# Performance work log

Hardware: AMD Instinct MI355X
Metric: run time of the kernel (lower is better)

The kernel has to match this reference:

```python
import jax, jax.numpy as jnp
import numpy as np

D, NH, L, P, FF = 256, 8, 3, 4, 1024
DH = D // NH
EPS = 1e-5

def _ln(x, g, b):
    m = jnp.mean(x, axis=-1, keepdims=True)
    v = jnp.mean((x - m) ** 2, axis=-1, keepdims=True)
    return (x - m) * jax.lax.rsqrt(v + EPS) * g + b

def _bilinear(value, loc, Hl, Wl):
    # value: [B,NH,Nl,DH]; loc (x,y) in [0,1]: [B,N,NH,P,2]; grid_sample align_corners=False, zero padding
    B, N = loc.shape[0], loc.shape[1]
    x = loc[..., 0] * Wl - 0.5
    y = loc[..., 1] * Hl - 0.5
    x0 = jnp.floor(x)
    y0 = jnp.floor(y)
    lx, ly = x - x0, y - y0
    x0 = x0.astype(jnp.int32)
    y0 = y0.astype(jnp.int32)

    def gather(xi, yi):
        valid = ((xi >= 0) & (xi < Wl) & (yi >= 0) & (yi < Hl)).astype(value.dtype)
        idx = jnp.clip(yi, 0, Hl - 1) * Wl + jnp.clip(xi, 0, Wl - 1)  # [B,N,NH,P]
        idx = idx.transpose(0, 2, 1, 3).reshape(B, NH, N * P, 1)
        v = jnp.take_along_axis(value, idx, axis=2)  # [B,NH,N*P,DH]
        v = v.reshape(B, NH, N, P, DH).transpose(0, 2, 1, 3, 4)  # [B,N,NH,P,DH]
        return v * valid[..., None]

    v00 = gather(x0, y0)
    v01 = gather(x0 + 1, y0)
    v10 = gather(x0, y0 + 1)
    v11 = gather(x0 + 1, y0 + 1)
    return (v00 * ((1 - lx) * (1 - ly))[..., None] + v01 * (lx * (1 - ly))[..., None]
            + v10 * ((1 - lx) * ly)[..., None] + v11 * (lx * ly)[..., None])

def _forward(query, p3, p4, p5, Wv, bv, Woff, boff, Wattn, battn, Wref, bref, Wo, bo,
             W1, b1, W2, b2, g1, be1, g2, be2, shapes):
    B, N, _ = query.shape
    off = (query @ Woff + boff).reshape(B, N, NH, L, P, 2)
    aw = jax.nn.softmax((query @ Wattn + battn).reshape(B, N, NH, L * P), axis=-1).reshape(B, N, NH, L, P)
    ref = jax.nn.sigmoid(query @ Wref + bref)[:, :, None, None, :]  # [B,N,1,1,2]
    out = jnp.zeros((B, N, NH, DH), query.dtype)
    for l, (feat, (Hl, Wl)) in enumerate(zip((p3, p4, p5), shapes)):
        val = (feat @ Wv + bv).reshape(B, Hl * Wl, NH, DH).transpose(0, 2, 1, 3)  # [B,NH,Nl,DH]
        loc = ref + off[:, :, :, l] / jnp.array([Wl, Hl], query.dtype)  # offsets normalized by (W,H)
        samp = _bilinear(val, loc, Hl, Wl)  # [B,N,NH,P,DH]
        out = out + jnp.einsum('bnhp,bnhpd->bnhd', aw[:, :, :, l], samp)
    attn_out = out.reshape(B, N, D) @ Wo + bo
    q = _ln(query + attn_out, g1, be1)  # residual + norm1 (dropout=eval identity)
    ffn = jax.nn.gelu(q @ W1 + b1, approximate=False) @ W2 + b2
    return _ln(q + ffn, g2, be2)

def setup_inputs():
    key = jax.random.key(0)
    ks = jax.random.split(key, 12)
    B = 4
    H3, W3, H4, W4, H5, W5 = 100, 100, 50, 50, 25, 25
    N = H3 * W3 + H4 * W4 + H5 * W5
    s = 0.02
    f32 = jnp.float32
    return dict(
        query=jax.random.normal(ks[0], (B, N, D), f32),
        p3=jax.random.normal(ks[1], (B, H3 * W3, D), f32),
        p4=jax.random.normal(ks[2], (B, H4 * W4, D), f32),
        p5=jax.random.normal(ks[3], (B, H5 * W5, D), f32),
        Wv=jax.random.normal(ks[4], (D, D), f32) * s, bv=jnp.zeros((D,), f32),
        Woff=jax.random.normal(ks[5], (D, NH * L * P * 2), f32) * s, boff=jnp.zeros((NH * L * P * 2,), f32),
        Wattn=jax.random.normal(ks[6], (D, NH * L * P), f32) * s, battn=jnp.zeros((NH * L * P,), f32),
        Wref=jax.random.normal(ks[7], (D, 2), f32) * s, bref=jnp.zeros((2,), f32),
        Wo=jax.random.normal(ks[8], (D, D), f32) * s, bo=jnp.zeros((D,), f32),
        W1=jax.random.normal(ks[9], (D, FF), f32) * s, b1=jnp.zeros((FF,), f32),
        W2=jax.random.normal(ks[10], (FF, D), f32) * s, b2=jnp.zeros((D,), f32),
        g1=jnp.ones((D,), f32), be1=jnp.zeros((D,), f32),
        g2=jnp.ones((D,), f32), be2=jnp.zeros((D,), f32),
        H3=H3, W3=W3, H4=H4, W4=W4, H5=H5, W5=W5,
    )

def reference(query, p3, p4, p5, Wv, bv, Woff, boff, Wattn, battn, Wref, bref, Wo, bo,
              W1, b1, W2, b2, g1, be1, g2, be2, H3, W3, H4, W4, H5, W5):
    return _forward(query, p3, p4, p5, Wv, bv, Woff, boff, Wattn, battn, Wref, bref, Wo, bo,
                    W1, b1, W2, b2, g1, be1, g2, be2, ((H3, W3), (H4, W4), (H5, W5)))
```

## Files before the change

### kernel.cpp

```cpp
#include <hip/hip_runtime.h>
#include <math.h>

#define BQ    4
#define NTOT  13125
#define DD    256
#define NHH   8
#define FFD   1024
#define EPSLN 1e-5f
#define MROWS (BQ * NTOT)
#define MPAD  52736

typedef __bf16 bf16_t;
typedef bf16_t bf16x8 __attribute__((ext_vector_type(8)));
typedef float floatx4 __attribute__((ext_vector_type(4)));

__device__ __forceinline__ unsigned short f2bf(float f) {
    unsigned u = __float_as_uint(f);
    return (unsigned short)((u + 0x7FFFu + ((u >> 16) & 1u)) >> 16);
}
__device__ __forceinline__ float bf2f(unsigned short h) {
    return __uint_as_float(((unsigned)h) << 16);
}

typedef const __attribute__((address_space(1))) unsigned int* gptr_t;
typedef __attribute__((address_space(3))) unsigned int* lptr_t;
__device__ __forceinline__ void gld16(const void* g, void* l) {
    __builtin_amdgcn_global_load_lds((gptr_t)g, (lptr_t)l, 16, 0, 0);
}

enum { EPI_F32 = 0, EPI_GELU = 2, EPI_VALSEG = 3 };

__device__ __forceinline__ int val_row(int gm) {
    if (gm < 40064) {
        if (gm >= 40000) return -1;
        int b = gm / 10000; int nl = gm - b * 10000;
        return b * NTOT + nl;
    } else if (gm < 50176) {
        int r = gm - 40064;
        if (r >= 10000) return -1;
        int b = r / 2500; int nl = r - b * 2500;
        return b * NTOT + 10000 + nl;
    } else {
        int r = gm - 50176;
        if (r >= 2500) return -1;
        int b = r / 625; int nl = r - b * 625;
        return b * NTOT + 12500 + nl;
    }
}

template <int EPI, typename OutT>
__launch_bounds__(256)
__global__ void mm_k(const unsigned short* __restrict__ A,
                     const unsigned short* __restrict__ Bt,
                     const float* __restrict__ bias, OutT* __restrict__ C,
                     int M, int K, int Nout, int ldc, int Mstore) {
    __shared__ __align__(16) unsigned short As[128 * 32];
    __shared__ __align__(16) unsigned short Bs[128 * 32];

    const int tid = threadIdx.x;
    const int m0 = blockIdx.x * 128;
    const int n0 = blockIdx.y * 128;
    const int w = tid >> 6, lane = tid & 63;
    const int q = lane >> 4, l15 = lane & 15;
    const int wm = (w & 1) * 64, wn = (w >> 1) * 64;

    const int sr = tid >> 2;
    const int sk = (tid & 3) * 8;

    const unsigned short* Ag = A + (size_t)(m0 + sr) * K + sk;
    const unsigned short* Bg = Bt + (size_t)(n0 + sr) * K + sk;
    char* AsB = (char*)As;
    char* BsB = (char*)Bs;

    floatx4 acc[4][4];
#pragma unroll
    for (int t = 0; t < 4; t++)
#pragma unroll
        for (int u = 0; u < 4; u++) {
            floatx4 z = {0.f, 0.f, 0.f, 0.f};
            acc[t][u] = z;
        }

    for (int k0 = 0; k0 < K; k0 += 32) {
        gld16(Ag + k0, AsB + tid * 16);
        gld16(Ag + (size_t)64 * K + k0, AsB + 4096 + tid * 16);
        gld16(Bg + k0, BsB + tid * 16);
        gld16(Bg + (size_t)64 * K + k0, BsB + 4096 + tid * 16);
        __syncthreads();

        bf16x8 af[4], bfr[4];
#pragma unroll
        for (int t = 0; t < 4; t++)
            af[t] = *reinterpret_cast<const bf16x8*>(&As[(wm + t * 16 + l15) * 32 + q * 8]);
#pragma unroll
        for (int u = 0; u < 4; u++)
            bfr[u] = *reinterpret_cast<const bf16x8*>(&Bs[(wn + u * 16 + l15) * 32 + q * 8]);
#pragma unroll
        for (int t = 0; t < 4; t++)
#pragma unroll
            for (int u = 0; u < 4; u++)
                acc[t][u] = __builtin_amdgcn_mfma_f32_16x16x32_bf16(af[t], bfr[u], acc[t][u], 0, 0, 0);
        __syncthreads();
    }

    float bias_v[4];
#pragma unroll
    for (int u = 0; u < 4; u++) {
        int gn = n0 + wn + u * 16 + l15;
        bias_v[u] = (gn < Nout) ? bias[gn] : 0.f;
    }

#pragma unroll
    for (int t = 0; t < 4; t++) {
#pragma unroll
        for (int r = 0; r < 4; r++) {
            int gm = m0 + wm + t * 16 + q * 4 + r;
            int orow = gm;
            if (EPI == EPI_VALSEG) orow = val_row(gm);
#pragma unroll
            for (int u = 0; u < 4; u++) {
                int gn = n0 + wn + u * 16 + l15;
                if (gn >= Nout) continue;
                float v = acc[t][u][r] + bias_v[u];
                if (EPI == EPI_GELU) {
                    v = 0.5f * v * (1.f + erff(v * 0.70710678118f));
                    if (gm < Mstore) {
                        float ov = (gm < M) ? v : 0.f;
                        ((unsigned short*)C)[(size_t)gm * ldc + gn] = f2bf(ov);
                    }
                } else if (EPI == EPI_VALSEG) {
                    if (orow >= 0)
                        ((unsigned short*)C)[(size_t)orow * ldc + gn] = f2bf(v);
                } else {
                    if (gm < M) ((float*)C)[(size_t)gm * ldc + gn] = v;
                }
            }
        }
    }
}

template <typename RT, typename OT>
__launch_bounds__(256)
__global__ void gemmln_k(const unsigned short* __restrict__ A,
                         const unsigned short* __restrict__ Bt,
                         const float* __restrict__ bias, const RT* __restrict__ res,
                         const float* __restrict__ g, const float* __restrict__ be,
                         OT* __restrict__ out, int M, int K) {
    __shared__ __align__(16) unsigned short As[64 * 32];
    __shared__ __align__(16) unsigned short Bs[256 * 32];

    const int tid = threadIdx.x;
    const int m0 = blockIdx.x * 64;
    const int w = tid >> 6, lane = tid & 63;
    const int q = lane >> 4, l15 = lane & 15;
    const int wn = w * 64;

    const int sr = tid >> 2;
    const int sk = (tid & 3) * 8;
    const unsigned short* Ag = A + (size_t)(m0 + sr) * K + sk;
    const unsigned short* Bg = Bt + (size_t)sr * K + sk;
    char* AsB = (char*)As;
    char* BsB = (char*)Bs;

    floatx4 acc[4][4];
#pragma unroll
    for (int t = 0; t < 4; t++)
#pragma unroll
        for (int u = 0; u < 4; u++) {
            floatx4 z = {0.f, 0.f, 0.f, 0.f};
            acc[t][u] = z;
        }

    for (int k0 = 0; k0 < K; k0 += 32) {
        gld16(Ag + k0, AsB + tid * 16);
#pragma unroll
        for (int j = 0; j < 4; j++)
            gld16(Bg + (size_t)j * 64 * K + k0, BsB + j * 4096 + tid * 16);
        __syncthreads();

        bf16x8 af[4], bfr[4];
#pragma unroll
        for (int t = 0; t < 4; t++)
            af[t] = *reinterpret_cast<const bf16x8*>(&As[(t * 16 + l15) * 32 + q * 8]);
#pragma unroll
        for (int u = 0; u < 4; u++)
            bfr[u] = *reinterpret_cast<const bf16x8*>(&Bs[(wn + u * 16 + l15) * 32 + q * 8]);
#pragma unroll
        for (int t = 0; t < 4; t++)
#pragma unroll
            for (int u = 0; u < 4; u++)
                acc[t][u] = __builtin_amdgcn_mfma_f32_16x16x32_bf16(af[t], bfr[u], acc[t][u], 0, 0, 0);
        __syncthreads();
    }

    float gg[4], bb[4], bias_v[4];
#pragma unroll
    for (int u = 0; u < 4; u++) {
        int gn = wn + u * 16 + l15;
        gg[u] = g[gn]; bb[u] = be[gn]; bias_v[u] = bias[gn];
    }

    float x[4][4][4];
    float ssum[4][4], ssq[4][4];
#pragma unroll
    for (int t = 0; t < 4; t++) {
#pragma unroll
        for (int r = 0; r < 4; r++) {
            int gm = m0 + t * 16 + q * 4 + r;
            bool valid = gm < M;
            float s = 0.f, sq = 0.f;
#pragma unroll
            for (int u = 0; u < 4; u++) {
                int gn = wn + u * 16 + l15;
                float rv = 0.f;
                if (valid) {
                    if (sizeof(RT) == 2)
                        rv = bf2f(((const unsigned short*)res)[(size_t)gm * DD + gn]);
                    else
                        rv = ((const float*)res)[(size_t)gm * DD + gn];
                }
                float xx = acc[t][u][r] + bias_v[u] + rv;
                x[t][r][u] = xx;
                s += xx; sq += xx * xx;
            }
            ssum[t][r] = s; ssq[t][r] = sq;
        }
    }
#pragma unroll
    for (int m = 1; m <= 8; m <<= 1) {
#pragma unroll
        for (int t = 0; t < 4; t++)
#pragma unroll
            for (int r = 0; r < 4; r++) {
                ssum[t][r] += __shfl_xor(ssum[t][r], m);
                ssq[t][r] += __shfl_xor(ssq[t][r], m);
            }
    }
    float* Ls = (float*)As;
    float* Lq = Ls + 256;
    if (l15 == 0) {
#pragma unroll
        for (int t = 0; t < 4; t++)
#pragma unroll
            for (int r = 0; r < 4; r++) {
                int lr = t * 16 + q * 4 + r;
                Ls[lr * 4 + w] = ssum[t][r];
                Lq[lr * 4 + w] = ssq[t][r];
            }
    }
    __syncthreads();

#pragma unroll
    for (int t = 0; t < 4; t++) {
#pragma unroll
        for (int r = 0; r < 4; r++) {
            int lr = t * 16 + q * 4 + r;
            int gm = m0 + lr;
            float tot = Ls[lr * 4 + 0] + Ls[lr * 4 + 1] + Ls[lr * 4 + 2] + Ls[lr * 4 + 3];
            float totq = Lq[lr * 4 + 0] + Lq[lr * 4 + 1] + Lq[lr * 4 + 2] + Lq[lr * 4 + 3];
            float mean = tot * (1.f / DD);
            float var = totq * (1.f / DD) - mean * mean;
            float rs = rsqrtf(var + EPSLN);
            if (gm < M) {
#pragma unroll
                for (int u = 0; u < 4; u++) {
                    int gn = wn + u * 16 + l15;
                    float o = (x[t][r][u] - mean) * rs * gg[u] + bb[u];
                    if (sizeof(OT) == 2)
                        ((unsigned short*)out)[(size_t)gm * DD + gn] = f2bf(o);
                    else
                        ((float*)out)[(size_t)gm * DD + gn] = o;
                }
            }
        }
    }
}

#define QELEMS   13500416
#define F3ELEMS  10256384
#define F4ELEMS   2588672
#define TOTELEMS 27000832

__launch_bounds__(256)
__global__ void cast_acts_k(const float* __restrict__ query, const float* __restrict__ p3,
                            const float* __restrict__ p4, const float* __restrict__ p5,
                            unsigned short* __restrict__ qbf, unsigned short* __restrict__ featsb) {
    int idx4 = (blockIdx.x * 256 + threadIdx.x) * 4;
    if (idx4 >= TOTELEMS) return;
    const float* src; unsigned short* dst; int local, real;
    if (idx4 < QELEMS) {
        src = query; dst = qbf; local = idx4; real = 13440000;
    } else {
        int j = idx4 - QELEMS;
        if (j < F3ELEMS)              { src = p3; dst = featsb;                    local = j;            real = 10240000; }
        else if (j < F3ELEMS + F4ELEMS){ src = p4; dst = featsb + F3ELEMS;         local = j - F3ELEMS;  real = 2560000; }
        else                          { src = p5; dst = featsb + F3ELEMS + F4ELEMS; local = j - F3ELEMS - F4ELEMS; real = 640000; }
    }
    float4 v = make_float4(0.f, 0.f, 0.f, 0.f);
    if (local < real) v = *(const float4*)&src[local];
    ushort4 o;
    o.x = f2bf(v.x); o.y = f2bf(v.y); o.z = f2bf(v.z); o.w = f2bf(v.w);
    *(ushort4*)&dst[local] = o;
}

#define WTQ_E   98304
#define WTV_E   (WTQ_E + 65536)
#define WTO_E   (WTV_E + 65536)
#define WT1_E   (WTO_E + 262144)
#define WT2_E   (WT1_E + 262144)
#define PREP_TOT (WT2_E + 384)

__launch_bounds__(256)
__global__ void prep_w_k(const float* __restrict__ Woff, const float* __restrict__ Wattn,
                         const float* __restrict__ Wref, const float* __restrict__ Wv,
                         const float* __restrict__ Wo, const float* __restrict__ W1,
                         const float* __restrict__ W2, const float* __restrict__ boff,
                         const float* __restrict__ battn, const float* __restrict__ bref,
                         unsigned short* __restrict__ warena, float* __restrict__ biasq) {
    int i = blockIdx.x * 256 + threadIdx.x;
    if (i >= PREP_TOT) return;
    if (i >= WT2_E) {
        int t = i - WT2_E;
        biasq[t] = (t < 192) ? boff[t] : (t < 288 ? battn[t - 192] : (t < 290 ? bref[t - 288] : 0.f));
        return;
    }
    float v;
    if (i < WTQ_E) {
        int n = i >> 8, k = i & 255;
        v = (n < 192) ? Woff[k * 192 + n]
          : (n < 288) ? Wattn[k * 96 + (n - 192)]
          : (n < 290) ? Wref[k * 2 + (n - 288)] : 0.f;
    } else if (i < WTV_E) {
        int j = i - WTQ_E; int n = j >> 8, k = j & 255;
        v = Wv[k * 256 + n];
    } else if (i < WTO_E) {
        int j = i - WTV_E; int n = j >> 8, k = j & 255;
        v = Wo[k * 256 + n];
    } else if (i < WT1_E) {
        int j = i - WTO_E; int n = j >> 8, k = j & 255;
        v = W1[k * 1024 + n];
    } else {
        int j = i - WT1_E; int n = j >> 10, k = j & 1023;
        v = W2[k * 256 + n];
    }
    warena[i] = f2bf(v);
}

__launch_bounds__(256)
__global__ void softmax12_k(const float* __restrict__ projb, unsigned short* __restrict__ aw) {
    int rh = blockIdx.x * 256 + threadIdx.x;
    if (rh >= MROWS * NHH) return;
    int bn = rh >> 3, h = rh & 7;
    const float* p = projb + (size_t)bn * 320 + 192 + h * 12;
    float v[12], mx = -1e30f;
#pragma unroll
    for (int i = 0; i < 12; i++) { v[i] = p[i]; mx = fmaxf(mx, v[i]); }
    float s = 0.f;
#pragma unroll
    for (int i = 0; i < 12; i++) { v[i] = expf(v[i] - mx); s += v[i]; }
    float inv = 1.f / s;
    unsigned short* o = aw + (size_t)rh * 12;
#pragma unroll
    for (int i = 0; i < 12; i++) o[i] = f2bf(v[i] * inv);
}

__launch_bounds__(128)
__global__ void sample_k(const unsigned short* __restrict__ val, const float* __restrict__ projb,
                         const unsigned short* __restrict__ aw,
                         unsigned short* __restrict__ out) {
    const int wv = threadIdx.x >> 6;
    const int lane = threadIdx.x & 63;
    const int bn = blockIdx.x * 2 + wv;
    const int b = bn / NTOT;
    __shared__ uint2 sc[2][96][4];

    const float* prow = projb + (size_t)bn * 320;
    float rx = 1.f / (1.f + expf(-prow[288]));
    float ry = 1.f / (1.f + expf(-prow[289]));
    for (int s0 = lane; s0 < 96; s0 += 64) {
        const int lp = s0 % 12;
        const int l = lp >> 2;
        int Hl, Wl, loff;
        if (l == 0)      { Hl = 100; Wl = 100; loff = 0; }
        else if (l == 1) { Hl = 50;  Wl = 50;  loff = 10000; }
        else             { Hl = 25;  Wl = 25;  loff = 12500; }
        float ox = prow[s0 * 2 + 0];
        float oy = prow[s0 * 2 + 1];
        float a  = bf2f(aw[(size_t)bn * 96 + s0]);
        float x = rx * (float)Wl + ox - 0.5f;
        float y = ry * (float)Hl + oy - 0.5f;
        x = fminf(fmaxf(x, -1e4f), 1e4f);
        y = fminf(fmaxf(y, -1e4f), 1e4f);
        float x0f = floorf(x), y0f = floorf(y);
        float lx = x - x0f, ly = y - y0f;
        int x0 = (int)x0f, y0 = (int)y0f;
#pragma unroll
        for (int c = 0; c < 4; c++) {
            int xi = x0 + (c & 1);
            int yi = y0 + (c >> 1);
            bool ok = (xi >= 0) && (xi < Wl) && (yi >= 0) && (yi < Hl);
            int xc = min(max(xi, 0), Wl - 1);
            int yc = min(max(yi, 0), Hl - 1);
            int idx = b * NTOT + loff + yc * Wl + xc;
            float wgt = ((c & 1) ? lx : 1.f - lx) * ((c >> 1) ? ly : 1.f - ly);
            sc[wv][s0][c] = make_uint2(__float_as_uint(ok ? a * wgt : 0.f), (unsigned)(idx * 512));
        }
    }
    __syncthreads();

    const int h = lane >> 3;
    const int dq = (lane & 7) * 4;
    const char* vb = (const char*)val + h * 64 + dq * 2;
    float a0 = 0.f, a1 = 0.f, a2 = 0.f, a3 = 0.f;
#pragma unroll
    for (int lp = 0; lp < 12; lp++) {
        int s = h * 12 + lp;
#pragma unroll
        for (int c = 0; c < 4; c++) {
            uint2 p = sc[wv][s][c];
            float wgt = __uint_as_float(p.x);
            uint2 u = *(const uint2*)(vb + p.y);
            a0 += wgt * __uint_as_float(u.x << 16);
            a1 += wgt * __uint_as_float(u.x & 0xFFFF0000u);
            a2 += wgt * __uint_as_float(u.y << 16);
            a3 += wgt * __uint_as_float(u.y & 0xFFFF0000u);
        }
    }
    uint2 ov;
    ov.x = (unsigned)f2bf(a0) | ((unsigned)f2bf(a1) << 16);
    ov.y = (unsigned)f2bf(a2) | ((unsigned)f2bf(a3) << 16);
    *(uint2*)(out + (size_t)bn * DD + h * 32 + dq) = ov;
}

extern "C" void kernel_launch(void* const* d_in, const int* in_sizes, int n_in,
                              void* d_out, int out_size, void* d_ws, size_t ws_size,
                              hipStream_t stream) {
    const float* query = (const float*)d_in[0];
    const float* p3    = (const float*)d_in[1];
    const float* p4    = (const float*)d_in[2];
    const float* p5    = (const float*)d_in[3];
    const float* Wv    = (const float*)d_in[4];
    const float* bv    = (const float*)d_in[5];
    const float* Woff  = (const float*)d_in[6];
    const float* boff  = (const float*)d_in[7];
    const float* Wattn = (const float*)d_in[8];
    const float* battn = (const float*)d_in[9];
    const float* Wref  = (const float*)d_in[10];
    const float* bref  = (const float*)d_in[11];
    const float* Wo    = (const float*)d_in[12];
    const float* bo    = (const float*)d_in[13];
    const float* W1    = (const float*)d_in[14];
    const float* b1    = (const float*)d_in[15];
    const float* W2    = (const float*)d_in[16];
    const float* b2    = (const float*)d_in[17];
    const float* g1    = (const float*)d_in[18];
    const float* be1   = (const float*)d_in[19];
    const float* g2    = (const float*)d_in[20];
    const float* be2   = (const float*)d_in[21];
    float* outp = (float*)d_out;

    char* wsb = (char*)d_ws;
    unsigned short* qbf    = (unsigned short*)(wsb + 0);
    float*          projb  = (float*)(wsb + 27000832);
    unsigned short* awb    = (unsigned short*)(wsb + 94502912);
    unsigned short* featsb = (unsigned short*)(wsb + 104582912);
    unsigned short* valb   = (unsigned short*)(wsb + 131583744);
    unsigned short* sampb  = (unsigned short*)(wsb + 158463744);
    unsigned short* warena = (unsigned short*)(wsb + 185399296);
    float*          biasq  = (float*)(wsb + 186906624);
    unsigned short* hidb   = (unsigned short*)(wsb + 27000832);

    unsigned short* Wtq = warena;
    unsigned short* Wtv = warena + WTQ_E;
    unsigned short* Wto = warena + WTV_E;
    unsigned short* Wt1 = warena + WTO_E;
    unsigned short* Wt2 = warena + WT1_E;

    cast_acts_k<<<dim3(TOTELEMS / 4 / 256), 256, 0, stream>>>(query, p3, p4, p5, qbf, featsb);
    prep_w_k<<<dim3((PREP_TOT + 255) / 256), 256, 0, stream>>>(
        Woff, Wattn, Wref, Wv, Wo, W1, W2, boff, battn, bref, warena, biasq);
    mm_k<EPI_F32, float><<<dim3(MPAD / 128, 3), 256, 0, stream>>>(
        qbf, Wtq, biasq, projb, MROWS, 256, 290, 320, 0);
    softmax12_k<<<dim3((MROWS * NHH + 255) / 256), 256, 0, stream>>>(projb, awb);
    mm_k<EPI_VALSEG, unsigned short><<<dim3(MPAD / 128, 2), 256, 0, stream>>>(
        featsb, Wtv, bv, valb, 0, 256, 256, 256, 0);
    sample_k<<<dim3(MROWS / 2), 128, 0, stream>>>(valb, projb, awb, sampb);
    gemmln_k<float, unsigned short><<<dim3((MROWS + 63) / 64), 256, 0, stream>>>(
        sampb, Wto, bo, query, g1, be1, qbf, MROWS, 256);
    mm_k<EPI_GELU, unsigned short><<<dim3(MPAD / 128, FFD / 128), 256, 0, stream>>>(
        qbf, Wt1, b1, hidb, MROWS, 256, FFD, FFD, MPAD);
    gemmln_k<unsigned short, float><<<dim3((MROWS + 63) / 64), 256, 0, stream>>>(
        hidb, Wt2, b2, qbf, g2, be2, outp, MROWS, 1024);
}
```

Baseline: 598.6 us.

## Add fused FFN kernel keeping GELU hidden activations in shared memory

Adds a kernel that computes W1 GEMM, bias+GELU, W2 GEMM, residual add and LayerNorm for a 64-row tile in one pass. The hidden activations are staged chunk by chunk in swizzled LDS and never go to global memory. This is meant to remove the round trip of the 1024-wide hidden tensor and the extra kernel launches. No host code calling the new kernel is visible, so it may not be used yet.

```diff
diff --git a/kernel.cpp b/kernel.cpp
--- a/kernel.cpp
+++ b/kernel.cpp
@@ -270,6 +270,182 @@
                         ((unsigned short*)out)[(size_t)gm * DD + gn] = f2bf(o);
                     else
                         ((float*)out)[(size_t)gm * DD + gn] = o;
+                }
+            }
+        }
+    }
+}
+
+__launch_bounds__(256)
+__global__ void ffn_k(const unsigned short* __restrict__ A,
+                      const unsigned short* __restrict__ Wt1,
+                      const float* __restrict__ b1,
+                      const unsigned short* __restrict__ Wt2,
+                      const float* __restrict__ b2,
+                      const float* __restrict__ g, const float* __restrict__ be,
+                      float* __restrict__ out, int M) {
+    __shared__ __align__(16) unsigned short qs[8 * 64 * 32];
+    __shared__ __align__(16) unsigned short Hs[64 * 128];
+
+    const int tid = threadIdx.x;
+    const int m0 = blockIdx.x * 64;
+    const int w = tid >> 6, lane = tid & 63;
+    const int q = lane >> 4, l15 = lane & 15;
+    const int wn1 = w * 32;
+    const int wn2 = w * 64;
+
+    {
+        const int sr = tid >> 2;
+        const int sk = (tid & 3) * 8;
+        const unsigned short* Ag = A + (size_t)(m0 + sr) * 256 + sk;
+        char* qsB = (char*)qs;
+#pragma unroll
+        for (int p = 0; p < 8; p++)
+            gld16(Ag + p * 32, qsB + p * 4096 + tid * 16);
+    }
+
+    floatx4 acc2[4][4];
+#pragma unroll
+    for (int t = 0; t < 4; t++)
+#pragma unroll
+        for (int u = 0; u < 4; u++) {
+            floatx4 z = {0.f, 0.f, 0.f, 0.f};
+            acc2[t][u] = z;
+        }
+
+    __syncthreads();
+
+#pragma unroll 1
+    for (int j = 0; j < 8; j++) {
+        floatx4 acc1[4][2];
+#pragma unroll
+        for (int t = 0; t < 4; t++)
+#pragma unroll
+            for (int u2 = 0; u2 < 2; u2++) {
+                floatx4 z = {0.f, 0.f, 0.f, 0.f};
+                acc1[t][u2] = z;
+            }
+        const unsigned short* W1p = Wt1 + (size_t)(j * 128 + wn1) * 256;
+#pragma unroll
+        for (int kk = 0; kk < 8; kk++) {
+            bf16x8 af[4], bf1[2];
+#pragma unroll
+            for (int t = 0; t < 4; t++)
+                af[t] = *reinterpret_cast<const bf16x8*>(&qs[kk * 2048 + (t * 16 + l15) * 32 + q * 8]);
+#pragma unroll
+            for (int u2 = 0; u2 < 2; u2++)
+                bf1[u2] = *reinterpret_cast<const bf16x8*>(&W1p[(size_t)(u2 * 16 + l15) * 256 + kk * 32 + q * 8]);
+#pragma unroll
+            for (int t = 0; t < 4; t++)
+#pragma unroll
+                for (int u2 = 0; u2 < 2; u2++)
+                    acc1[t][u2] = __builtin_amdgcn_mfma_f32_16x16x32_bf16(af[t], bf1[u2], acc1[t][u2], 0, 0, 0);
+        }
+        __syncthreads();
+#pragma unroll
+        for (int u2 = 0; u2 < 2; u2++) {
+            int col = wn1 + u2 * 16 + l15;
+            float bv = b1[j * 128 + col];
+#pragma unroll
+            for (int t = 0; t < 4; t++)
+#pragma unroll
+                for (int r = 0; r < 4; r++) {
+                    int row = t * 16 + q * 4 + r;
+                    float v = acc1[t][u2][r] + bv;
+                    v = 0.5f * v * (1.f + erff(v * 0.70710678118f));
+                    int bo = (row * 256 + col * 2) ^ ((row & 7) << 4);
+                    *(unsigned short*)((char*)Hs + bo) = f2bf(v);
+                }
+        }
+        __syncthreads();
+        const unsigned short* W2p = Wt2 + (size_t)wn2 * 1024 + j * 128;
+#pragma unroll
+        for (int kk2 = 0; kk2 < 4; kk2++) {
+            bf16x8 af2[4], bf2[4];
+#pragma unroll
+            for (int t = 0; t < 4; t++) {
+                int row = t * 16 + l15;
+                int bo = (row * 256 + (kk2 * 32 + q * 8) * 2) ^ ((row & 7) << 4);
+                af2[t] = *reinterpret_cast<const bf16x8*>((const char*)Hs + bo);
+            }
+#pragma unroll
+            for (int u = 0; u < 4; u++)
+                bf2[u] = *reinterpret_cast<const bf16x8*>(&W2p[(size_t)(u * 16 + l15) * 1024 + kk2 * 32 + q * 8]);
+#pragma unroll
+            for (int t = 0; t < 4; t++)
+#pragma unroll
+                for (int u = 0; u < 4; u++)
+                    acc2[t][u] = __builtin_amdgcn_mfma_f32_16x16x32_bf16(af2[t], bf2[u], acc2[t][u], 0, 0, 0);
+        }
+    }
+
+    float gg[4], bb[4], bias_v[4];
+#pragma unroll
+    for (int u = 0; u < 4; u++) {
+        int gn = wn2 + u * 16 + l15;
+        gg[u] = g[gn]; bb[u] = be[gn]; bias_v[u] = b2[gn];
+    }
+
+    float x[4][4][4];
+    float ssum[4][4], ssq[4][4];
+#pragma unroll
+    for (int t = 0; t < 4; t++) {
+#pragma unroll
+        for (int r = 0; r < 4; r++) {
+            int row = t * 16 + q * 4 + r;
+            float s = 0.f, sq = 0.f;
+#pragma unroll
+            for (int u = 0; u < 4; u++) {
+                int gn = wn2 + u * 16 + l15;
+                float rv = bf2f(qs[(gn >> 5) * 2048 + row * 32 + (gn & 31)]);
+                float xx = acc2[t][u][r] + bias_v[u] + rv;
+                x[t][r][u] = xx;
+                s += xx; sq += xx * xx;
+            }
+            ssum[t][r] = s; ssq[t][r] = sq;
+        }
+    }
+#pragma unroll
+    for (int m = 1; m <= 8; m <<= 1) {
+#pragma unroll
+        for (int t = 0; t < 4; t++)
+#pragma unroll
+            for (int r = 0; r < 4; r++) {
+                ssum[t][r] += __shfl_xor(ssum[t][r], m);
+                ssq[t][r] += __shfl_xor(ssq[t][r], m);
+            }
+    }
+    __syncthreads();
+    float* Ls = (float*)qs;
+    float* Lq = Ls + 256;
+    if (l15 == 0) {
+#pragma unroll
+        for (int t = 0; t < 4; t++)
+#pragma unroll
+            for (int r = 0; r < 4; r++) {
+                int lr = t * 16 + q * 4 + r;
+                Ls[lr * 4 + w] = ssum[t][r];
+                Lq[lr * 4 + w] = ssq[t][r];
+            }
+    }
+    __syncthreads();
+
+#pragma unroll
+    for (int t = 0; t < 4; t++) {
+#pragma unroll
+        for (int r = 0; r < 4; r++) {
+            int lr = t * 16 + q * 4 + r;
+            int gm = m0 + lr;
+            float tot = Ls[lr * 4 + 0] + Ls[lr * 4 + 1] + Ls[lr * 4 + 2] + Ls[lr * 4 + 3];
+            float totq = Lq[lr * 4 + 0] + Lq[lr * 4 + 1] + Lq[lr * 4 + 2] + Lq[lr * 4 + 3];
+            float mean = tot * (1.f / DD);
+            float var = totq * (1.f / DD) - mean * mean;
+            float rs = rsqrtf(var + EPSLN);
+            if (gm < M) {
+#pragma unroll
+                for (int u = 0; u < 4; u++) {
+                    int gn = wn2 + u * 16 + l15;
+                    out[(size_t)gm * DD + gn] = (x[t][r][u] - mean) * rs * gg[u] + bb[u];
                 }
             }
         }
```

Measured after the change: 595.5 us. Within noise of the previous version (-0.5%).
